# Performance work log

Hardware: AMD Instinct MI355X
Metric: run time of the kernel (lower is better)

The kernel has to match this reference:

```python
import jax, jax.numpy as jnp
import numpy as np

HEADS = 4
ATTN_MODE = 'strided'
LOCAL_ATTN_CTX = 32
BLOCKSIZE = 32


def strided_transpose(x, n_ctx, local_attn_ctx):
    # [n, t, e] -> [n, bT_ctx, local, e] -> [n, local, bT_ctx, e] -> [n, t, e]
    bT_ctx = n_ctx // local_attn_ctx
    n, t, e = x.shape
    x = x.reshape(n, bT_ctx, local_attn_ctx, e)
    x = jnp.transpose(x, (0, 2, 1, 3))
    return x.reshape(n, t, e)


def setup_inputs() -> dict:
    key = jax.random.key(0)
    kq, kk, kv = jax.random.split(key, 3)
    shape = (2, 4096, 1024)
    return {
        'q': jax.random.normal(kq, shape, dtype=jnp.float32),
        'k': jax.random.normal(kk, shape, dtype=jnp.float32),
        'v': jax.random.normal(kv, shape, dtype=jnp.float32),
    }


def reference(q, k, v):
    n_ctx = q.shape[1]
    if ATTN_MODE == 'strided':
        bT_ctx = n_ctx // LOCAL_ATTN_CTX
        assert bT_ctx % BLOCKSIZE == 0
        q = strided_transpose(q, n_ctx, LOCAL_ATTN_CTX)
        k = strided_transpose(k, n_ctx, LOCAL_ATTN_CTX)
        v = strided_transpose(v, n_ctx, LOCAL_ATTN_CTX)
    n_state = q.shape[-1] // HEADS
    scale = 1.0 / np.sqrt(n_state)
    w = jnp.einsum('nte,nse->nts', q, k)            # [n, t, t] full scores
    w = jax.nn.softmax(w * scale, axis=-1)
    a = jnp.einsum('nts,nse->nte', w, v)
    if ATTN_MODE == 'strided':
        n, t, e = a.shape
        bT_ctx = n_ctx // LOCAL_ATTN_CTX
        a = a.reshape(n, LOCAL_ATTN_CTX, bT_ctx, e)
        a = jnp.transpose(a, (0, 2, 1, 3))
        a = a.reshape(n, t, e)
    return a
```

## Files before the change

kernel.cpp:

```cpp
#include <hip/hip_runtime.h>

using short8  = __attribute__((ext_vector_type(8))) short;
using ushort8 = __attribute__((ext_vector_type(8))) unsigned short;
using f32x4   = __attribute__((ext_vector_type(4))) float;

#define T 4096
#define E 1024
#define NB 2
#define BM 128
#define BN 128
#define BK 32
#define TILE_ELEMS (BM * BK)
#define TILE_A_W   (256 * BK)

__device__ __forceinline__ unsigned short f2bf(float f) {
    unsigned int u = __builtin_bit_cast(unsigned int, f);
    u = (u + 0x7FFFu + ((u >> 16) & 1u)) >> 16;
    return (unsigned short)u;
}

__device__ __forceinline__ void gld16(const unsigned short* g, unsigned short* l) {
    __builtin_amdgcn_global_load_lds(
        (__attribute__((address_space(1))) void*)g,
        (__attribute__((address_space(3))) void*)l, 16, 0, 0);
}

__device__ __forceinline__ void do_cvt(const float* __restrict__ src,
                                       unsigned short* __restrict__ dst, int blk) {
    size_t i = ((size_t)blk * 256 + threadIdx.x) * 8;
    float4 f0 = *(const float4*)(src + i);
    float4 f1 = *(const float4*)(src + i + 4);
    ushort8 u;
    u[0]=f2bf(f0.x); u[1]=f2bf(f0.y); u[2]=f2bf(f0.z); u[3]=f2bf(f0.w);
    u[4]=f2bf(f1.x); u[5]=f2bf(f1.y); u[6]=f2bf(f1.z); u[7]=f2bf(f1.w);
    *(ushort8*)(dst + i) = u;
}

__device__ __forceinline__ void do_vt(const float* __restrict__ v,
                                      unsigned short* __restrict__ vt, int id,
                                      float (*tile)[65], int tid) {
    int b   = id / (64 * 16);
    int rem = id % (64 * 16);
    int t0  = (rem / 16) * 64;
    int e0  = (rem % 16) * 64;
    int r   = tid >> 2;
    int c0  = (tid & 3) * 16;
    const float* src = v + ((size_t)(b * T + t0 + r)) * E + e0 + c0;
    #pragma unroll
    for (int i = 0; i < 4; i++) {
        float4 f = *(const float4*)(src + i * 4);
        tile[r][c0 + i*4 + 0] = f.x;
        tile[r][c0 + i*4 + 1] = f.y;
        tile[r][c0 + i*4 + 2] = f.z;
        tile[r][c0 + i*4 + 3] = f.w;
    }
    __syncthreads();
    int er = tid >> 2;
    #pragma unroll
    for (int ch = 0; ch < 2; ch++) {
        int tl = (tid & 3) * 16 + ch * 8;
        ushort8 u;
        #pragma unroll
        for (int j = 0; j < 8; j++) u[j] = f2bf(tile[tl + j][er]);
        *(ushort8*)(vt + ((size_t)(b * E + e0 + er)) * T + t0 + tl) = u;
    }
}

__global__ __launch_bounds__(256) void prologue(const float* __restrict__ q,
                                                const float* __restrict__ k,
                                                unsigned short* __restrict__ qb,
                                                unsigned short* __restrict__ kb,
                                                float* __restrict__ lsum) {
    int bid = blockIdx.x;
    if (bid < 4096)      do_cvt(q, qb, bid);
    else if (bid < 8192) do_cvt(k, kb, bid - 4096);
    else                 lsum[(bid - 8192) * 256 + threadIdx.x] = 0.0f;
}
__global__ __launch_bounds__(256) void v_transpose(const float* __restrict__ v,
                                                   unsigned short* __restrict__ vt) {
    __shared__ float tile[64][65];
    do_vt(v, vt, blockIdx.x, tile, threadIdx.x);
}

template <int KITERS>
__device__ __forceinline__ void gemm_core64(const unsigned short* Abase, int apitch,
                                            const unsigned short* Bbase, int bpitch,
                                            unsigned short* ldsA, unsigned short* ldsB,
                                            int tid, f32x4 (&acc)[4][4]) {
    constexpr int TILE64 = 128 * 64;
    const int lane = tid & 63, wave = tid >> 6;
    const int l15 = lane & 15, kq = lane >> 4;
    const int wm = (wave & 1) * 64, wn = (wave >> 1) * 64;

    int goA[4], goB[4], lo[4];
    #pragma unroll
    for (int i = 0; i < 4; i++) {
        int p = i * 256 + tid;
        int r = p >> 3, c = p & 7;
        int sw = c ^ (r & 7);
        goA[i] = r * apitch + sw * 8;
        goB[i] = r * bpitch + sw * 8;
        lo[i] = (i * 256 + wave * 64) * 8;
    }
    int aoff[2][4], boff[2][4];
    #pragma unroll
    for (int mi = 0; mi < 4; mi++) {
        int r = wm + mi * 16 + l15;
        aoff[0][mi] = (r * 8 + (kq ^ (r & 7))) * 8;
        aoff[1][mi] = (r * 8 + ((kq ^ 4) ^ (r & 7))) * 8;
        int rn = wn + mi * 16 + l15;
        boff[0][mi] = (rn * 8 + (kq ^ (rn & 7))) * 8;
        boff[1][mi] = (rn * 8 + ((kq ^ 4) ^ (rn & 7))) * 8;
    }

    #pragma unroll
    for (int i = 0; i < 4; i++) gld16(Abase + goA[i], ldsA + lo[i]);
    #pragma unroll
    for (int i = 0; i < 4; i++) gld16(Bbase + goB[i], ldsB + lo[i]);

    int cbuf = 0;
    for (int kt = 0; kt < KITERS; kt++) {
        int pk = (kt + 1 < KITERS) ? (kt + 1) : 0;
        int ob = cbuf ^ 1;
        asm volatile("s_barrier" ::: "memory");
        #pragma unroll
        for (int i = 0; i < 4; i++) gld16(Abase + goA[i] + pk * 64, ldsA + ob * TILE64 + lo[i]);
        #pragma unroll
        for (int i = 0; i < 4; i++) gld16(Bbase + goB[i] + pk * 64, ldsB + ob * TILE64 + lo[i]);
        asm volatile("s_waitcnt vmcnt(8)" ::: "memory");
        asm volatile("s_barrier" ::: "memory");

        const unsigned short* A = ldsA + cbuf * TILE64;
        const unsigned short* B = ldsB + cbuf * TILE64;
        #pragma unroll
        for (int ks = 0; ks < 2; ks++) {
            short8 af[4], bf[4];
            #pragma unroll
            for (int i = 0; i < 4; i++) {
                af[i] = *(const short8*)(A + aoff[ks][i]);
                bf[i] = *(const short8*)(B + boff[ks][i]);
            }
            #pragma unroll
            for (int mi = 0; mi < 4; mi++)
                #pragma unroll
                for (int ni = 0; ni < 4; ni++)
                    acc[mi][ni] = __builtin_amdgcn_mfma_f32_16x16x32_bf16(af[mi], bf[ni], acc[mi][ni], 0, 0, 0);
        }
        cbuf = ob;
    }
}

template <int KITERS>
__device__ __forceinline__ void gemm_core_wide(const unsigned short* Abase, int apitch,
                                               const unsigned short* Bbase, int bpitch,
                                               unsigned short* ldsA, unsigned short* ldsB,
                                               int tid, f32x4 (&acc)[4][4]) {
    const int lane = tid & 63, wave = tid >> 6;
    const int l15 = lane & 15, kq = lane >> 4;
    const int wm = (wave & 3) * 64, wn = (wave >> 2) * 64;

    const unsigned short* ga[2];
    int lao[2];
    #pragma unroll
    for (int i = 0; i < 2; i++) {
        int p = i * 512 + tid;
        int r = p >> 2;
        int kqw = (p & 3) ^ ((p >> 3) & 3);
        ga[i] = Abase + (size_t)r * apitch + kqw * 8;
        lao[i] = (i * 512 + wave * 64) * 8;
    }
    const unsigned short* gb;
    int lbo;
    {
        int p = tid;
        int r = p >> 2;
        int kqw = (p & 3) ^ ((p >> 3) & 3);
        gb = Bbase + (size_t)r * bpitch + kqw * 8;
        lbo = (wave * 64) * 8;
    }
    int aoff[4], boff[4];
    #pragma unroll
    for (int mi = 0; mi < 4; mi++) {
        int r = wm + mi * 16 + l15;
        aoff[mi] = (r * 4 + (kq ^ ((r >> 1) & 3))) * 8;
        int rn = wn + mi * 16 + l15;
        boff[mi] = (rn * 4 + (kq ^ ((rn >> 1) & 3))) * 8;
    }

    gld16(ga[0], ldsA + lao[0]);
    gld16(ga[1], ldsA + lao[1]);
    gld16(gb,    ldsB + lbo);

    int cbuf = 0;
    for (int kt = 0; kt < KITERS; kt++) {
        int nxt = (kt + 1 < KITERS) ? (kt + 1) : 0;
        int obuf = cbuf ^ 1;
        asm volatile("s_barrier" ::: "memory");
        gld16(ga[0] + nxt * BK, ldsA + obuf * TILE_A_W + lao[0]);
        gld16(ga[1] + nxt * BK, ldsA + obuf * TILE_A_W + lao[1]);
        gld16(gb    + nxt * BK, ldsB + obuf * TILE_ELEMS + lbo);
        asm volatile("s_waitcnt vmcnt(3)" ::: "memory");
        asm volatile("s_barrier" ::: "memory");

        const unsigned short* A = ldsA + cbuf * TILE_A_W;
        const unsigned short* B = ldsB + cbuf * TILE_ELEMS;
        short8 af[4], bf[4];
        #pragma unroll
        for (int i = 0; i < 4; i++) {
            af[i] = *(const short8*)(A + aoff[i]);
            bf[i] = *(const short8*)(B + boff[i]);
        }
        #pragma unroll
        for (int mi = 0; mi < 4; mi++)
            #pragma unroll
            for (int ni = 0; ni < 4; ni++)
                acc[mi][ni] = __builtin_amdgcn_mfma_f32_16x16x32_bf16(af[mi], bf[ni], acc[mi][ni], 0, 0, 0);

        cbuf = obuf;
    }
}

__global__ __launch_bounds__(512, 2) void pass1(const unsigned short* __restrict__ qb,
                                                const unsigned short* __restrict__ kb,
                                                const float* __restrict__ v,
                                                unsigned short* __restrict__ vt,
                                                unsigned short* __restrict__ P,
                                                float* __restrict__ lsum) {
    __shared__ unsigned short lds[2 * TILE_A_W + 2 * TILE_ELEMS];
    const int bx = blockIdx.x;
    const int tid = threadIdx.x;

    if (bx >= 1024) {
        const int vb = bx - 1024;
        float (*tileA)[65] = (float (*)[65])lds;
        float (*tileB)[65] = (float (*)[65])(lds + 8320);
        if (tid < 256) do_vt(v, vt, vb * 2,     tileA, tid);
        else           do_vt(v, vt, vb * 2 + 1, tileB, tid - 256);
        return;
    }

    unsigned short* ldsA = lds;
    unsigned short* ldsB = lds + 2 * TILE_A_W;
    const int x = bx & 7, j = bx >> 3;
    const int gm = x * 4 + (j & 3);
    const int nt = j >> 2;
    const int b = gm >> 4, mt = gm & 15;

    f32x4 acc[4][4];
    #pragma unroll
    for (int i = 0; i < 4; i++)
        #pragma unroll
        for (int jj = 0; jj < 4; jj++) acc[i][jj] = {};

    gemm_core_wide<E / BK>(qb + ((size_t)b * T + mt * 256) * E, E,
                           kb + ((size_t)b * T + nt * BN) * E, E,
                           ldsA, ldsB, tid, acc);

    const int lane = tid & 63, wave = tid >> 6;
    const int wm = (wave & 3) * 64, wn = (wave >> 2) * 64;
    const int quad = lane >> 4, l15 = lane & 15;
    const float sl2 = 0.0625f * 1.44269504089f;
    const int col0 = nt * BN + wn + l15;

    #pragma unroll
    for (int mi = 0; mi < 4; mi++) {
        #pragma unroll
        for (int r = 0; r < 4; r++) {
            int row = mt * 256 + wm + mi * 16 + quad * 4 + r;
            size_t base = ((size_t)b * T + row) * T + col0;
            float s = 0.0f;
            #pragma unroll
            for (int ni = 0; ni < 4; ni++) {
                float p = exp2f(acc[mi][ni][r] * sl2 - 12.0f);
                P[base + ni * 16] = f2bf(p);
                s += p;
            }
            s += __shfl_xor(s, 1);
            s += __shfl_xor(s, 2);
            s += __shfl_xor(s, 4);
            s += __shfl_xor(s, 8);
            if (l15 == 0) atomicAdd(lsum + b * T + row, s);
        }
    }
}

__global__ __launch_bounds__(256, 2) void pass2(const unsigned short* __restrict__ P,
                                                const unsigned short* __restrict__ vt,
                                                const float* __restrict__ lsum,
                                                float* __restrict__ out) {
    constexpr int TILE64 = 128 * 64;
    __shared__ unsigned short ldsA[2 * TILE64];
    __shared__ unsigned short ldsB[2 * TILE64];

    const int bx = blockIdx.x;
    const int x = bx & 7, j = bx >> 3;
    const int gm = x * 8 + (j & 7);
    const int nt = j >> 3;
    const int b = gm >> 5, mt = gm & 31;
    const int tid = threadIdx.x;

    f32x4 acc[4][4];
    #pragma unroll
    for (int i = 0; i < 4; i++)
        #pragma unroll
        for (int jj = 0; jj < 4; jj++) acc[i][jj] = {};

    gemm_core64<T / 64>(P + ((size_t)b * T + mt * 128) * T, T,
                        vt + ((size_t)b * E + nt * 128) * T, T,
                        ldsA, ldsB, tid, acc);

    const int lane = tid & 63, wave = tid >> 6;
    const int wm = (wave & 1) * 64, wn = (wave >> 1) * 64;
    const int quad = lane >> 4, l15 = lane & 15;
    const int col0 = nt * 128 + wn + l15;

    #pragma unroll
    for (int mi = 0; mi < 4; mi++) {
        #pragma unroll
        for (int r = 0; r < 4; r++) {
            int row = mt * 128 + wm + mi * 16 + quad * 4 + r;
            float rl = 1.0f / lsum[b * T + row];
            size_t base = ((size_t)b * T + row) * E + col0;
            #pragma unroll
            for (int ni = 0; ni < 4; ni++)
                out[base + ni * 16] = acc[mi][ni][r] * rl;
        }
    }
}

extern "C" void kernel_launch(void* const* d_in, const int* in_sizes, int n_in,
                              void* d_out, int out_size, void* d_ws, size_t ws_size,
                              hipStream_t stream) {
    const float* q = (const float*)d_in[0];
    const float* k = (const float*)d_in[1];
    const float* v = (const float*)d_in[2];
    float* out = (float*)d_out;

    const size_t QK = (size_t)NB * T * E;
    const size_t PSZ = (size_t)NB * T * T;
    float* lsum = (float*)d_ws;
    unsigned short* qbw = (unsigned short*)((char*)d_ws + 32768);
    unsigned short* kbw = qbw + QK;
    unsigned short* Pw  = kbw + QK;

    const size_t full_need = 32768 + (3 * QK + PSZ) * sizeof(unsigned short);

    if (ws_size >= full_need) {
        unsigned short* vtw = Pw + PSZ;
        prologue<<<8224, 256, 0, stream>>>(q, k, qbw, kbw, lsum);
        pass1<<<1024 + 1024, 512, 0, stream>>>(qbw, kbw, v, vtw, Pw, lsum);
        pass2<<<512, 256, 0, stream>>>(Pw, vtw, lsum, out);
    } else {
        unsigned short* vtw = qbw;
        prologue<<<8224, 256, 0, stream>>>(q, k, qbw, kbw, lsum);
        pass1<<<1024, 512, 0, stream>>>(qbw, kbw, v, vtw, Pw, lsum);
        v_transpose<<<NB * 64 * 16, 256, 0, stream>>>(v, vtw);
        pass2<<<512, 256, 0, stream>>>(Pw, vtw, lsum, out);
    }
}
```

Measured before the change: 284.3 us.

## Fuse K fp32-to-bf16 conversion into the QK GEMM B-tile load

Drops the separate K conversion from the prologue. Inside the QK^T GEMM, fp32 K rows are read from global memory, converted to bf16 with packed v_cvt_pk_bf16_f32 instructions, and written to the swizzled LDS B tile through registers, replacing the direct global-to-LDS load of the bf16 copy. This saves a full K read/write round trip and shrinks the prologue. The cost is twice the global bytes for K in every pass1 tile that reuses it, plus an extra barrier and register staging in the inner loop. It also reorders the fallback path so v_transpose runs before pass1 into the freed kb buffer.

```diff
diff --git a/kernel.cpp b/kernel.cpp
--- a/kernel.cpp
+++ b/kernel.cpp
@@ -3,6 +3,7 @@
 using short8  = __attribute__((ext_vector_type(8))) short;
 using ushort8 = __attribute__((ext_vector_type(8))) unsigned short;
 using f32x4   = __attribute__((ext_vector_type(4))) float;
+using uint4v  = __attribute__((ext_vector_type(4))) unsigned int;
 
 #define T 4096
 #define E 1024
@@ -17,6 +18,15 @@
     unsigned int u = __builtin_bit_cast(unsigned int, f);
     u = (u + 0x7FFFu + ((u >> 16) & 1u)) >> 16;
     return (unsigned short)u;
+}
+
+__device__ __forceinline__ uint4v cvt8(float4 a, float4 b) {
+    uint4v u;
+    asm("v_cvt_pk_bf16_f32 %0, %1, %2" : "=v"(u[0]) : "v"(a.x), "v"(a.y));
+    asm("v_cvt_pk_bf16_f32 %0, %1, %2" : "=v"(u[1]) : "v"(a.z), "v"(a.w));
+    asm("v_cvt_pk_bf16_f32 %0, %1, %2" : "=v"(u[2]) : "v"(b.x), "v"(b.y));
+    asm("v_cvt_pk_bf16_f32 %0, %1, %2" : "=v"(u[3]) : "v"(b.z), "v"(b.w));
+    return u;
 }
 
 __device__ __forceinline__ void gld16(const unsigned short* g, unsigned short* l) {
@@ -67,14 +77,11 @@
 }
 
 __global__ __launch_bounds__(256) void prologue(const float* __restrict__ q,
-                                                const float* __restrict__ k,
                                                 unsigned short* __restrict__ qb,
-                                                unsigned short* __restrict__ kb,
                                                 float* __restrict__ lsum) {
     int bid = blockIdx.x;
-    if (bid < 4096)      do_cvt(q, qb, bid);
-    else if (bid < 8192) do_cvt(k, kb, bid - 4096);
-    else                 lsum[(bid - 8192) * 256 + threadIdx.x] = 0.0f;
+    if (bid < 4096) do_cvt(q, qb, bid);
+    else            lsum[(bid - 4096) * 256 + threadIdx.x] = 0.0f;
 }
 __global__ __launch_bounds__(256) void v_transpose(const float* __restrict__ v,
                                                    unsigned short* __restrict__ vt) {
@@ -152,7 +159,7 @@
 
 template <int KITERS>
 __device__ __forceinline__ void gemm_core_wide(const unsigned short* Abase, int apitch,
-                                               const unsigned short* Bbase, int bpitch,
+                                               const float* Bf, int bpitch,
                                                unsigned short* ldsA, unsigned short* ldsB,
                                                int tid, f32x4 (&acc)[4][4]) {
     const int lane = tid & 63, wave = tid >> 6;
@@ -169,14 +176,11 @@
         ga[i] = Abase + (size_t)r * apitch + kqw * 8;
         lao[i] = (i * 512 + wave * 64) * 8;
     }
-    const unsigned short* gb;
-    int lbo;
+    const float* gbf; int bwo;
     {
-        int p = tid;
-        int r = p >> 2;
-        int kqw = (p & 3) ^ ((p >> 3) & 3);
-        gb = Bbase + (size_t)r * bpitch + kqw * 8;
-        lbo = (wave * 64) * 8;
+        int r = tid >> 2, h = tid & 3;
+        gbf = Bf + (size_t)r * bpitch + h * 8;
+        bwo = (r * 4 + (h ^ ((r >> 1) & 3))) * 8;
     }
     int aoff[4], boff[4];
     #pragma unroll
@@ -189,39 +193,48 @@
 
     gld16(ga[0], ldsA + lao[0]);
     gld16(ga[1], ldsA + lao[1]);
-    gld16(gb,    ldsB + lbo);
+    {
+        float4 b0 = *(const float4*)(gbf);
+        float4 b1 = *(const float4*)(gbf + 4);
+        *(uint4v*)(ldsB + bwo) = cvt8(b0, b1);
+    }
+    __syncthreads();
 
     int cbuf = 0;
     for (int kt = 0; kt < KITERS; kt++) {
         int nxt = (kt + 1 < KITERS) ? (kt + 1) : 0;
         int obuf = cbuf ^ 1;
-        asm volatile("s_barrier" ::: "memory");
+        float4 b0 = *(const float4*)(gbf + nxt * BK);
+        float4 b1 = *(const float4*)(gbf + nxt * BK + 4);
         gld16(ga[0] + nxt * BK, ldsA + obuf * TILE_A_W + lao[0]);
         gld16(ga[1] + nxt * BK, ldsA + obuf * TILE_A_W + lao[1]);
-        gld16(gb    + nxt * BK, ldsB + obuf * TILE_ELEMS + lbo);
-        asm volatile("s_waitcnt vmcnt(3)" ::: "memory");
+        asm volatile("s_waitcnt vmcnt(4)" ::: "memory");
         asm volatile("s_barrier" ::: "memory");
 
         const unsigned short* A = ldsA + cbuf * TILE_A_W;
         const unsigned short* B = ldsB + cbuf * TILE_ELEMS;
-        short8 af[4], bf[4];
+        short8 af[4], bfr[4];
         #pragma unroll
         for (int i = 0; i < 4; i++) {
-            af[i] = *(const short8*)(A + aoff[i]);
-            bf[i] = *(const short8*)(B + boff[i]);
+            af[i]  = *(const short8*)(A + aoff[i]);
+            bfr[i] = *(const short8*)(B + boff[i]);
         }
         #pragma unroll
         for (int mi = 0; mi < 4; mi++)
             #pragma unroll
             for (int ni = 0; ni < 4; ni++)
-                acc[mi][ni] = __builtin_amdgcn_mfma_f32_16x16x32_bf16(af[mi], bf[ni], acc[mi][ni], 0, 0, 0);
-
+                acc[mi][ni] = __builtin_amdgcn_mfma_f32_16x16x32_bf16(af[mi], bfr[ni], acc[mi][ni], 0, 0, 0);
+
+        asm volatile("s_waitcnt vmcnt(2)" ::: "memory");
+        *(uint4v*)(ldsB + obuf * TILE_ELEMS + bwo) = cvt8(b0, b1);
+        asm volatile("s_waitcnt lgkmcnt(0)" ::: "memory");
+        asm volatile("s_barrier" ::: "memory");
         cbuf = obuf;
     }
 }
 
 __global__ __launch_bounds__(512, 2) void pass1(const unsigned short* __restrict__ qb,
-                                                const unsigned short* __restrict__ kb,
+                                                const float* __restrict__ kf,
                                                 const float* __restrict__ v,
                                                 unsigned short* __restrict__ vt,
                                                 unsigned short* __restrict__ P,
@@ -253,7 +266,7 @@
         for (int jj = 0; jj < 4; jj++) acc[i][jj] = {};
 
     gemm_core_wide<E / BK>(qb + ((size_t)b * T + mt * 256) * E, E,
-                           kb + ((size_t)b * T + nt * BN) * E, E,
+                           kf + ((size_t)b * T + nt * BN) * E, E,
                            ldsA, ldsB, tid, acc);
 
     const int lane = tid & 63, wave = tid >> 6;
@@ -347,14 +360,14 @@
 
     if (ws_size >= full_need) {
         unsigned short* vtw = Pw + PSZ;
-        prologue<<<8224, 256, 0, stream>>>(q, k, qbw, kbw, lsum);
-        pass1<<<1024 + 1024, 512, 0, stream>>>(qbw, kbw, v, vtw, Pw, lsum);
+        prologue<<<4128, 256, 0, stream>>>(q, qbw, lsum);
+        pass1<<<2048, 512, 0, stream>>>(qbw, k, v, vtw, Pw, lsum);
         pass2<<<512, 256, 0, stream>>>(Pw, vtw, lsum, out);
     } else {
-        unsigned short* vtw = qbw;
-        prologue<<<8224, 256, 0, stream>>>(q, k, qbw, kbw, lsum);
-        pass1<<<1024, 512, 0, stream>>>(qbw, kbw, v, vtw, Pw, lsum);
+        unsigned short* vtw = kbw;
+        prologue<<<4128, 256, 0, stream>>>(q, qbw, lsum);
         v_transpose<<<NB * 64 * 16, 256, 0, stream>>>(v, vtw);
+        pass1<<<1024, 512, 0, stream>>>(qbw, k, v, vtw, Pw, lsum);
         pass2<<<512, 256, 0, stream>>>(Pw, vtw, lsum, out);
     }
 }
```

Result: slower. 301.6 us (+6.1%).
